# Optimization experiments

Hardware: AMD Instinct MI355X
Metric: run time of the kernel (lower is better)

The kernel has to match this reference:

```python
import jax, jax.numpy as jnp
import numpy as np

N = 8192
D = 128
LMBD = 0.1
SPARSITY = 0.99  # fraction of zero entries in A


def setup_inputs() -> dict:
    key = jax.random.key(0)
    kA, kW = jax.random.split(key)
    u = jax.random.uniform(kA, (N, N), dtype=jnp.float32)
    A = jnp.where(u > SPARSITY, u, 0.0)
    W = jax.random.normal(kW, (N, D), dtype=jnp.float32) * 0.02
    b = jnp.zeros((D,), dtype=jnp.float32)
    return {"A": A, "W": W, "b": b}


def reference(A, W, b):
    # model(tf.eye(N)) with Dense(d) == eye(N) @ W + b == W + b  -> [N, d]
    Y = W + b
    # main loss: 0.5 * sum(mask * (A - Y Y^T)^2), mask = (A > 0)
    R = A - jnp.matmul(Y, Y.T)  # [N, N]
    main_loss = 0.5 * jnp.sum(jnp.where(A > 0, R * R, 0.0))
    # reg loss: lmbd/2 * ||Y||_F^2
    reg_loss = 0.5 * LMBD * jnp.sum(Y * Y)
    return main_loss + reg_loss
```

## Files before the change

### kernel.cpp

```cpp
#include <hip/hip_runtime.h>

#define N 8192
#define D 128

typedef __attribute__((ext_vector_type(8))) short short8;
typedef __attribute__((ext_vector_type(4))) float float4v;

__device__ __forceinline__ unsigned short f32_to_bf16(float f) {
    unsigned int u = __float_as_uint(f);
    unsigned int r = (u + 0x7fffu + ((u >> 16) & 1u)) >> 16;
    return (unsigned short)r;
}

__device__ __forceinline__ float wave_reduce(float p) {
    #pragma unroll
    for (int off = 32; off > 0; off >>= 1)
        p += __shfl_xor(p, off, 64);
    return p;
}

__global__ __launch_bounds__(256)
void gf_prep_kernel(const float* __restrict__ W, const float* __restrict__ b,
                    unsigned short* __restrict__ ybf, float* __restrict__ regp) {
    __shared__ float s_ws[4];
    const int t = blockIdx.x * 256 + threadIdx.x;
    const int f = t * 4;
    const int dcol = f & (D - 1);
    const float4 wv = *(const float4*)(W + f);
    const float4 bv = *(const float4*)(b + dcol);
    const float y0 = wv.x + bv.x, y1 = wv.y + bv.y, y2 = wv.z + bv.z, y3 = wv.w + bv.w;

    ushort4 o;
    o.x = f32_to_bf16(y0); o.y = f32_to_bf16(y1);
    o.z = f32_to_bf16(y2); o.w = f32_to_bf16(y3);
    *(ushort4*)(ybf + f) = o;

    float s = y0*y0 + y1*y1 + y2*y2 + y3*y3;
    s = wave_reduce(s);
    const int lane = threadIdx.x & 63, w = threadIdx.x >> 6;
    if (lane == 0) s_ws[w] = s;
    __syncthreads();
    if (threadIdx.x == 0)
        regp[blockIdx.x] = 0.05f * (s_ws[0] + s_ws[1] + s_ws[2] + s_ws[3]);
}

__global__ __launch_bounds__(256, 4)
void gf_sddmm_kernel(const float* __restrict__ A,
                     const unsigned short* __restrict__ ybf,
                     float* __restrict__ partials) {
    __shared__ float s_c[4][16][132];
    __shared__ float s_ws[4];

    const int lane = threadIdx.x & 63;
    const int w    = threadIdx.x >> 6;
    const int j0   = blockIdx.x * 128;
    const int i0   = blockIdx.y * 128 + w * 32;
    const int r16  = lane & 15;
    const int quad = lane >> 4;
    const int l32  = lane & 31;
    const int half = lane >> 5;

    short8 afr[2][4];
    #pragma unroll
    for (int s = 0; s < 2; ++s) {
        const unsigned short* yrow = ybf + (size_t)(i0 + s * 16 + r16) * D;
        #pragma unroll
        for (int c = 0; c < 4; ++c)
            afr[s][c] = *(const short8*)(yrow + c * 32 + quad * 8);
    }

    float loss = 0.0f;
    #pragma unroll
    for (int s = 0; s < 2; ++s) {
        float4 av[8];
        #pragma unroll
        for (int t = 0; t < 8; ++t) {
            const int m = 2 * t + half;
            av[t] = *(const float4*)(A + (size_t)(i0 + s * 16 + m) * N + j0 + l32 * 4);
        }
        #pragma unroll
        for (int jj = 0; jj < 8; ++jj) {
            const int jbase = j0 + jj * 16;
            short8 bfr[4];
            const unsigned short* yrow = ybf + (size_t)(jbase + r16) * D;
            #pragma unroll
            for (int c = 0; c < 4; ++c)
                bfr[c] = *(const short8*)(yrow + c * 32 + quad * 8);
            float4v acc = {0.f, 0.f, 0.f, 0.f};
            #pragma unroll
            for (int c = 0; c < 4; ++c)
                acc = __builtin_amdgcn_mfma_f32_16x16x32_bf16(afr[s][c], bfr[c], acc, 0, 0, 0);
            #pragma unroll
            for (int r = 0; r < 4; ++r)
                s_c[w][quad * 4 + r][jj * 16 + r16] = acc[r];
        }
        #pragma unroll
        for (int t = 0; t < 8; ++t) {
            const int m = 2 * t + half;
            const float4 cv = *(const float4*)&s_c[w][m][l32 * 4];
            float d;
            d = av[t].x - cv.x; loss += (av[t].x > 0.0f) ? d * d : 0.0f;
            d = av[t].y - cv.y; loss += (av[t].y > 0.0f) ? d * d : 0.0f;
            d = av[t].z - cv.z; loss += (av[t].z > 0.0f) ? d * d : 0.0f;
            d = av[t].w - cv.w; loss += (av[t].w > 0.0f) ? d * d : 0.0f;
        }
    }

    loss = wave_reduce(loss);
    if (lane == 0) s_ws[w] = loss;
    __syncthreads();
    if (threadIdx.x == 0)
        partials[blockIdx.y * gridDim.x + blockIdx.x] =
            0.5f * (s_ws[0] + s_ws[1] + s_ws[2] + s_ws[3]);
}

__global__ __launch_bounds__(256)
void gf_reduce_kernel(const float* __restrict__ parts, float* __restrict__ out) {
    __shared__ float s_ws[4];
    const int lane = threadIdx.x & 63, w = threadIdx.x >> 6;
    float s = 0.0f;
    for (int i = threadIdx.x; i < 4096 + 1024; i += 256) s += parts[i];
    s = wave_reduce(s);
    if (lane == 0) s_ws[w] = s;
    __syncthreads();
    if (threadIdx.x == 0) out[0] = s_ws[0] + s_ws[1] + s_ws[2] + s_ws[3];
}

extern "C" void kernel_launch(void* const* d_in, const int* in_sizes, int n_in,
                              void* d_out, int out_size, void* d_ws, size_t ws_size,
                              hipStream_t stream) {
    const float* A = (const float*)d_in[0];
    const float* W = (const float*)d_in[1];
    const float* b = (const float*)d_in[2];
    float* out = (float*)d_out;

    float* parts = (float*)d_ws;
    unsigned short* ybf = (unsigned short*)((float*)d_ws + 8192);

    gf_prep_kernel<<<dim3(N * D / 1024), dim3(256), 0, stream>>>(W, b, ybf, parts + 4096);
    gf_sddmm_kernel<<<dim3(64, 64), dim3(256), 0, stream>>>(A, ybf, parts);
    gf_reduce_kernel<<<dim3(1), dim3(256), 0, stream>>>(parts, out);
}
```

Before: 418.7 us.

## Split fused SDDMM into bf16 GEMM materialization and streaming loss kernel

Replaces the fused kernel that computed Y·Yᵀ tiles and the masked loss together with two kernels. One writes the full product matrix in bf16 to workspace, and a grid-stride kernel streams A and the product to compute the masked squared error. The aim is to decouple MFMA work from the A streaming so each runs with a simpler access pattern. In exchange it adds a large intermediate write and read, and rounds the product to bf16 before the subtraction.

```diff
diff --git a/kernel.cpp b/kernel.cpp
--- a/kernel.cpp
+++ b/kernel.cpp
@@ -45,11 +45,9 @@
 }
 
 __global__ __launch_bounds__(256, 4)
-void gf_sddmm_kernel(const float* __restrict__ A,
-                     const unsigned short* __restrict__ ybf,
-                     float* __restrict__ partials) {
+void gf_gemm_kernel(const unsigned short* __restrict__ ybf,
+                    unsigned short* __restrict__ C) {
     __shared__ float s_c[4][16][132];
-    __shared__ float s_ws[4];
 
     const int lane = threadIdx.x & 63;
     const int w    = threadIdx.x >> 6;
@@ -69,15 +67,8 @@
             afr[s][c] = *(const short8*)(yrow + c * 32 + quad * 8);
     }
 
-    float loss = 0.0f;
     #pragma unroll
     for (int s = 0; s < 2; ++s) {
-        float4 av[8];
-        #pragma unroll
-        for (int t = 0; t < 8; ++t) {
-            const int m = 2 * t + half;
-            av[t] = *(const float4*)(A + (size_t)(i0 + s * 16 + m) * N + j0 + l32 * 4);
-        }
         #pragma unroll
         for (int jj = 0; jj < 8; ++jj) {
             const int jbase = j0 + jj * 16;
@@ -98,20 +89,44 @@
         for (int t = 0; t < 8; ++t) {
             const int m = 2 * t + half;
             const float4 cv = *(const float4*)&s_c[w][m][l32 * 4];
-            float d;
-            d = av[t].x - cv.x; loss += (av[t].x > 0.0f) ? d * d : 0.0f;
-            d = av[t].y - cv.y; loss += (av[t].y > 0.0f) ? d * d : 0.0f;
-            d = av[t].z - cv.z; loss += (av[t].z > 0.0f) ? d * d : 0.0f;
-            d = av[t].w - cv.w; loss += (av[t].w > 0.0f) ? d * d : 0.0f;
+            ushort4 o;
+            o.x = f32_to_bf16(cv.x); o.y = f32_to_bf16(cv.y);
+            o.z = f32_to_bf16(cv.z); o.w = f32_to_bf16(cv.w);
+            *(ushort4*)(C + (size_t)(i0 + s * 16 + m) * N + j0 + l32 * 4) = o;
         }
     }
+}
 
-    loss = wave_reduce(loss);
-    if (lane == 0) s_ws[w] = loss;
+__global__ __launch_bounds__(256)
+void gf_loss_kernel(const float4* __restrict__ A4,
+                    const ushort4* __restrict__ C4,
+                    float* __restrict__ partials) {
+    __shared__ float s_ws[4];
+    const int tid    = blockIdx.x * 256 + threadIdx.x;
+    const int stride = gridDim.x * 256;
+
+    float acc = 0.0f;
+    #pragma unroll 2
+    for (int idx = tid; idx < N * N / 4; idx += stride) {
+        const float4  a = A4[idx];
+        const ushort4 c = C4[idx];
+        const float c0 = __uint_as_float((unsigned)c.x << 16);
+        const float c1 = __uint_as_float((unsigned)c.y << 16);
+        const float c2 = __uint_as_float((unsigned)c.z << 16);
+        const float c3 = __uint_as_float((unsigned)c.w << 16);
+        float d;
+        d = a.x - c0; acc += (a.x > 0.0f) ? d * d : 0.0f;
+        d = a.y - c1; acc += (a.y > 0.0f) ? d * d : 0.0f;
+        d = a.z - c2; acc += (a.z > 0.0f) ? d * d : 0.0f;
+        d = a.w - c3; acc += (a.w > 0.0f) ? d * d : 0.0f;
+    }
+
+    acc = wave_reduce(acc);
+    const int lane = threadIdx.x & 63, w = threadIdx.x >> 6;
+    if (lane == 0) s_ws[w] = acc;
     __syncthreads();
     if (threadIdx.x == 0)
-        partials[blockIdx.y * gridDim.x + blockIdx.x] =
-            0.5f * (s_ws[0] + s_ws[1] + s_ws[2] + s_ws[3]);
+        partials[blockIdx.x] = 0.5f * (s_ws[0] + s_ws[1] + s_ws[2] + s_ws[3]);
 }
 
 __global__ __launch_bounds__(256)
@@ -119,7 +134,7 @@
     __shared__ float s_ws[4];
     const int lane = threadIdx.x & 63, w = threadIdx.x >> 6;
     float s = 0.0f;
-    for (int i = threadIdx.x; i < 4096 + 1024; i += 256) s += parts[i];
+    for (int i = threadIdx.x; i < 2048 + 1024; i += 256) s += parts[i];
     s = wave_reduce(s);
     if (lane == 0) s_ws[w] = s;
     __syncthreads();
@@ -134,10 +149,14 @@
     const float* b = (const float*)d_in[2];
     float* out = (float*)d_out;
 
-    float* parts = (float*)d_ws;
-    unsigned short* ybf = (unsigned short*)((float*)d_ws + 8192);
+    char* ws = (char*)d_ws;
+    float* parts          = (float*)ws;
+    unsigned short* ybf   = (unsigned short*)(ws + 32768);
+    unsigned short* Cbuf  = (unsigned short*)(ws + 32768 + 2097152);
 
-    gf_prep_kernel<<<dim3(N * D / 1024), dim3(256), 0, stream>>>(W, b, ybf, parts + 4096);
-    gf_sddmm_kernel<<<dim3(64, 64), dim3(256), 0, stream>>>(A, ybf, parts);
+    gf_prep_kernel<<<dim3(N * D / 1024), dim3(256), 0, stream>>>(W, b, ybf, parts + 2048);
+    gf_gemm_kernel<<<dim3(64, 64), dim3(256), 0, stream>>>(ybf, Cbuf);
+    gf_loss_kernel<<<dim3(2048), dim3(256), 0, stream>>>((const float4*)A,
+                                                         (const ushort4*)Cbuf, parts);
     gf_reduce_kernel<<<dim3(1), dim3(256), 0, stream>>>(parts, out);
 }
```

Result: slower. 509.5 us (+21.7%).
